# Kernel optimization log

Measured on AMD Instinct MI355X. Metric: run time of the kernel, lower is better.

Reference implementation:

```python
import jax, jax.numpy as jnp
import numpy as np

B, S, HID, NH = 4, 1024, 1024, 16
HD = HID // NH  # 64


def setup_inputs() -> dict:
    key = jax.random.key(0)
    ks = jax.random.split(key, 8)
    scale = 0.02
    return {
        "attention_mask": jnp.zeros((B, 1, 1, S), dtype=jnp.float32),
        "query": jax.random.normal(ks[0], (B, S, HID), dtype=jnp.float32),
        "key": jax.random.normal(ks[1], (B, S, HID), dtype=jnp.float32),
        "value": jax.random.normal(ks[2], (B, S, HID), dtype=jnp.float32),
        "Wq": jax.random.normal(ks[3], (HID, HID), dtype=jnp.float32) * scale,
        "bq": jnp.zeros((HID,), dtype=jnp.float32),
        "Wk": jax.random.normal(ks[4], (HID, HID), dtype=jnp.float32) * scale,
        "bk": jnp.zeros((HID,), dtype=jnp.float32),
    }


def reference(attention_mask, query, key, value, Wq, bq, Wk, bk):
    # Linear projections (torch Linear: x @ W.T + b)
    q = query @ Wq.T + bq  # [B,S,HID]
    k = key @ Wk.T + bk    # [B,S,HID]
    # split heads -> [B,NH,S,HD]
    q = q.reshape(B, S, NH, HD).transpose(0, 2, 1, 3)
    k = k.reshape(B, S, NH, HD).transpose(0, 2, 1, 3)
    scores = jnp.einsum("bhqd,bhkd->bhqk", q, k) / jnp.sqrt(jnp.float32(HD))
    scores = scores + attention_mask  # additive mask broadcast [B,1,1,S]
    probs = jax.nn.softmax(scores, axis=-1)  # [B,NH,S,S]
    # V is shared across heads; head-mean folds into a single contraction:
    # mean_h(probs_h @ V) = (sum_h probs_h) @ V / NH
    out = jnp.einsum("bhqk,bkv->bqv", probs, value) / NH  # [B,S,HID]
    return out
```

## Files before the change

kernel.cpp:

```cpp
#include <hip/hip_runtime.h>
#include <hip/hip_fp16.h>

#define B_    4
#define S_    1024
#define HID_  1024
#define NH_   16
#define HD_   64

#define LOG2E 1.44269504f
#define PSTR  40

typedef _Float16 half8 __attribute__((ext_vector_type(8)));
typedef float f32x4 __attribute__((ext_vector_type(4)));

__device__ __forceinline__ half8 cvt8(float4 a, float4 b) {
    half8 h;
    h[0] = (_Float16)a.x; h[1] = (_Float16)a.y;
    h[2] = (_Float16)a.z; h[3] = (_Float16)a.w;
    h[4] = (_Float16)b.x; h[5] = (_Float16)b.y;
    h[6] = (_Float16)b.z; h[7] = (_Float16)b.w;
    return h;
}

__global__ __launch_bounds__(512) void proj_qk_f16(
    const float* __restrict__ query, const float* __restrict__ Wq,
    const float* __restrict__ bq, _Float16* __restrict__ Oq,
    const float* __restrict__ key, const float* __restrict__ Wk,
    const float* __restrict__ bk, _Float16* __restrict__ Ok)
{
    const int f  = blockIdx.x + 8 * blockIdx.y + 256 * blockIdx.z;
    const int w2 = (f & 7) * 64 + (f >> 3);
    const int bx = w2 & 7, by = (w2 >> 3) & 31, bz = w2 >> 8;

    const float* A    = bz ? key : query;
    const float* Wm   = bz ? Wk  : Wq;
    const float* bias = bz ? bk  : bq;
    _Float16* Co      = bz ? Ok  : Oq;

    __shared__ _Float16 Al[2][128 * PSTR];
    __shared__ _Float16 Bl[2][128 * PSTR];

    const int tid  = threadIdx.x;
    const int wv   = tid >> 6;
    const int lane = tid & 63;
    const int l15  = lane & 15;
    const int quad = lane >> 4;
    const int wm   = wv & 1, wn = wv >> 1;
    const int m0   = by * 128, n0 = bx * 128;
    const int sr   = tid >> 2;
    const int sc   = (tid & 3) * 8;

    const float* ap = A  + (long)(m0 + sr) * HID_ + sc;
    const float* bp = Wm + (long)(n0 + sr) * HID_ + sc;

    f32x4 acc[4][2];
#pragma unroll
    for (int i = 0; i < 4; i++)
#pragma unroll
        for (int j = 0; j < 2; j++) acc[i][j] = (f32x4){0.f, 0.f, 0.f, 0.f};

    float4 a0 = *(const float4*)ap,       a1 = *(const float4*)(ap + 4);
    float4 b0 = *(const float4*)bp,       b1 = *(const float4*)(bp + 4);
    *(half8*)&Al[0][sr * PSTR + sc] = cvt8(a0, a1);
    *(half8*)&Bl[0][sr * PSTR + sc] = cvt8(b0, b1);
    a0 = *(const float4*)(ap + 32); a1 = *(const float4*)(ap + 36);
    b0 = *(const float4*)(bp + 32); b1 = *(const float4*)(bp + 36);
    __syncthreads();

#pragma unroll 2
    for (int kt = 0; kt < HID_; kt += 32) {
        const int p = (kt >> 5) & 1;

        float4 na0 = a0, na1 = a1, nb0 = b0, nb1 = b1;
        if (kt + 64 < HID_) {
            na0 = *(const float4*)(ap + kt + 64);
            na1 = *(const float4*)(ap + kt + 68);
            nb0 = *(const float4*)(bp + kt + 64);
            nb1 = *(const float4*)(bp + kt + 68);
        }

        half8 af[4], bfm[2];
#pragma unroll
        for (int i = 0; i < 4; i++)
            af[i] = *(const half8*)(&Al[p][(wm * 64 + i * 16 + l15) * PSTR + quad * 8]);
#pragma unroll
        for (int j = 0; j < 2; j++)
            bfm[j] = *(const half8*)(&Bl[p][(wn * 32 + j * 16 + l15) * PSTR + quad * 8]);

        if (kt + 32 < HID_) {
            *(half8*)&Al[p ^ 1][sr * PSTR + sc] = cvt8(a0, a1);
            *(half8*)&Bl[p ^ 1][sr * PSTR + sc] = cvt8(b0, b1);
        }

#pragma unroll
        for (int i = 0; i < 4; i++)
#pragma unroll
            for (int j = 0; j < 2; j++)
                acc[i][j] = __builtin_amdgcn_mfma_f32_16x16x32_f16(
                    af[i], bfm[j], acc[i][j], 0, 0, 0);

        __syncthreads();
        a0 = na0; a1 = na1; b0 = nb0; b1 = nb1;
    }

    const int isQ = (bz == 0);
#pragma unroll
    for (int j = 0; j < 2; j++) {
        int col = n0 + wn * 32 + j * 16 + l15;
        float bv = bias[col];
        int h = col >> 6, d = col & 63, p = d >> 3, jj = d & 7;
#pragma unroll
        for (int i = 0; i < 4; i++) {
            int row = m0 + wm * 64 + i * 16 + quad * 4;
            int bb = row >> 10, ss = row & 1023;
            long base;
            if (isQ)
                base = ((((long)(bb * NH_ + h) * 64 + (ss >> 4)) * 8 + p) * 16
                        + (ss & 15)) * 8 + jj;
            else
                base = (((long)(bb * NH_ + h) * 8 + p) * 1024 + ss) * 8 + jj;
#pragma unroll
            for (int r = 0; r < 4; r++)
                Co[base + r * 8] = (_Float16)(acc[i][j][r] + bv);
        }
    }
}

__global__ __launch_bounds__(512) void attn_psum_f16(
    const _Float16* __restrict__ qb,
    const _Float16* __restrict__ kb,
    const float* __restrict__ mask,
    _Float16* __restrict__ P)
{
    const int b    = blockIdx.y;
    const int qt   = blockIdx.x;
    const int q0   = qt * 16;
    const int hz   = blockIdx.z;
    const int tid  = threadIdx.x;
    const int w    = tid >> 6;
    const int lane = tid & 63;
    const int l15  = lane & 15;
    const int quad = lane >> 4;

    __shared__ float redS[2][16][8];

    const float SC = 0.125f * LOG2E;

    float mreg[8];
#pragma unroll
    for (int t = 0; t < 8; t++)
        mreg[t] = mask[b * S_ + t * 128 + w * 16 + l15] * LOG2E;

    f32x4 acc[8];
#pragma unroll
    for (int t = 0; t < 8; t++) acc[t] = (f32x4){0.f, 0.f, 0.f, 0.f};

    for (int ii = 0; ii < 4; ii++) {
        const int h = hz * 4 + ii;
        const _Float16* qh = qb + ((long)(b * NH_ + h) * 64 + qt) * 1024;
        const _Float16* kh = kb + (long)(b * NH_ + h) * 8192 * 8;

        half8 a0 = *(const half8*)(qh + quad * 128 + l15 * 8);
        half8 a1 = *(const half8*)(qh + (quad + 4) * 128 + l15 * 8);

        f32x4 s[8];
#pragma unroll
        for (int cc = 0; cc < 8; cc++) {
            const int key = cc * 128 + w * 16 + l15;
            half8 b0 = *(const half8*)(kh + (long)quad * 8192 + key * 8);
            half8 b1 = *(const half8*)(kh + (long)(quad + 4) * 8192 + key * 8);
            f32x4 c = (f32x4){0.f, 0.f, 0.f, 0.f};
            c = __builtin_amdgcn_mfma_f32_16x16x32_f16(a0, b0, c, 0, 0, 0);
            c = __builtin_amdgcn_mfma_f32_16x16x32_f16(a1, b1, c, 0, 0, 0);
            s[cc] = c;
        }

        const int p = ii & 1;
        float sm[4] = {0.f, 0.f, 0.f, 0.f};
#pragma unroll
        for (int t = 0; t < 8; t++)
#pragma unroll
            for (int r = 0; r < 4; r++) {
                float pr = exp2f(s[t][r] * SC + mreg[t]);
                s[t][r] = pr;
                sm[r] += pr;
            }
#pragma unroll
        for (int off = 1; off < 16; off <<= 1)
#pragma unroll
            for (int r = 0; r < 4; r++) sm[r] += __shfl_xor(sm[r], off);
        if (l15 == 0)
#pragma unroll
            for (int r = 0; r < 4; r++) redS[p][quad * 4 + r][w] = sm[r];
        __syncthreads();

#pragma unroll
        for (int r = 0; r < 4; r++) {
            float4 v0 = *(float4*)&redS[p][quad * 4 + r][0];
            float4 v1 = *(float4*)&redS[p][quad * 4 + r][4];
            float tot = (v0.x + v0.y + v0.z + v0.w) + (v1.x + v1.y + v1.z + v1.w);
            float inv = 1.f / tot;
#pragma unroll
            for (int t = 0; t < 8; t++) acc[t][r] += s[t][r] * inv;
        }
    }

    _Float16* prow = P + (long)hz * ((long)B_ * S_ * S_) + (long)(b * S_ + q0) * S_;
#pragma unroll
    for (int t = 0; t < 8; t++)
#pragma unroll
        for (int r = 0; r < 4; r++) {
            int row = quad * 4 + r;
            prow[(long)row * S_ + t * 128 + w * 16 + l15] = (_Float16)acc[t][r];
        }
}

__global__ __launch_bounds__(256) void vt_combine(
    const _Float16* __restrict__ P, _Float16* __restrict__ o,
    const float* __restrict__ V, _Float16* __restrict__ Vt)
{
    __shared__ float t[32][33];
    if (blockIdx.y == 0) {
        if (blockIdx.x >= 2048) return;
        const long QS = (long)B_ * S_ * S_;
        long i = (long)(blockIdx.x * 256 + threadIdx.x) * 8;
        half8 a = *(const half8*)(P + i);
        half8 b = *(const half8*)(P + QS + i);
        half8 c = *(const half8*)(P + 2 * QS + i);
        half8 d = *(const half8*)(P + 3 * QS + i);
        half8 r;
#pragma unroll
        for (int e = 0; e < 8; e++)
            r[e] = (_Float16)((float)a[e] + (float)b[e] + (float)c[e] + (float)d[e]);
        *(half8*)(o + i) = r;
    } else {
        const int x  = blockIdx.x;
        const int b  = x >> 10;
        const int s0 = ((x >> 5) & 31) * 32;
        const int h0 = (x & 31) * 32;
        const int tx = threadIdx.x & 31, ty = threadIdx.x >> 5;
#pragma unroll
        for (int rr = 0; rr < 4; rr++) {
            int s = s0 + ty + rr * 8;
            t[ty + rr * 8][tx] = V[((long)b * S_ + s) * HID_ + h0 + tx];
        }
        __syncthreads();
#pragma unroll
        for (int rr = 0; rr < 4; rr++) {
            int h = h0 + ty + rr * 8;
            Vt[((long)b * HID_ + h) * S_ + s0 + tx] = (_Float16)t[tx][ty + rr * 8];
        }
    }
}

__global__ __launch_bounds__(256) void pv_f16(
    const _Float16* __restrict__ Pc,
    const _Float16* __restrict__ Vt,
    float* __restrict__ out)
{
    const int b = blockIdx.z;
    const _Float16* A  = Pc + (long)b * S_ * S_;
    const _Float16* Bm = Vt + (long)b * HID_ * S_;

    __shared__ _Float16 Al[128 * PSTR];
    __shared__ _Float16 Bl[64 * PSTR];

    const int tid  = threadIdx.x;
    const int wv   = tid >> 6;
    const int lane = tid & 63;
    const int l15  = lane & 15;
    const int quad = lane >> 4;
    const int wm   = wv & 1, wn = wv >> 1;
    const int m0   = blockIdx.y * 128, n0 = blockIdx.x * 64;
    const int sr   = tid >> 2;
    const int sc   = (tid & 3) * 8;

    f32x4 acc[4][2];
#pragma unroll
    for (int i = 0; i < 4; i++)
#pragma unroll
        for (int j = 0; j < 2; j++) acc[i][j] = (f32x4){0.f, 0.f, 0.f, 0.f};

    for (int kt = 0; kt < S_; kt += 32) {
        half8 a0 = *(const half8*)(A  + (long)(m0 + sr) * S_ + kt + sc);
        half8 a1 = *(const half8*)(A  + (long)(m0 + 64 + sr) * S_ + kt + sc);
        half8 b0 = *(const half8*)(Bm + (long)(n0 + sr) * S_ + kt + sc);
        __syncthreads();
        *(half8*)(Al + sr * PSTR + sc) = a0;
        *(half8*)(Al + (64 + sr) * PSTR + sc) = a1;
        *(half8*)(Bl + sr * PSTR + sc) = b0;
        __syncthreads();

        half8 af[4], bfm[2];
#pragma unroll
        for (int i = 0; i < 4; i++)
            af[i] = *(const half8*)(Al + (wm * 64 + i * 16 + l15) * PSTR + quad * 8);
#pragma unroll
        for (int j = 0; j < 2; j++)
            bfm[j] = *(const half8*)(Bl + (wn * 32 + j * 16 + l15) * PSTR + quad * 8);
#pragma unroll
        for (int i = 0; i < 4; i++)
#pragma unroll
            for (int j = 0; j < 2; j++)
                acc[i][j] = __builtin_amdgcn_mfma_f32_16x16x32_f16(
                    af[i], bfm[j], acc[i][j], 0, 0, 0);
    }

    const float alpha = 1.f / NH_;
#pragma unroll
    for (int i = 0; i < 4; i++) {
        int row = m0 + wm * 64 + i * 16 + quad * 4;
#pragma unroll
        for (int j = 0; j < 2; j++) {
            int col = n0 + wn * 32 + j * 16 + l15;
#pragma unroll
            for (int r = 0; r < 4; r++)
                out[(long)(b * S_ + row + r) * HID_ + col] = acc[i][j][r] * alpha;
        }
    }
}

extern "C" void kernel_launch(void* const* d_in, const int* in_sizes, int n_in,
                              void* d_out, int out_size, void* d_ws, size_t ws_size,
                              hipStream_t stream)
{
    const float* mask  = (const float*)d_in[0];
    const float* query = (const float*)d_in[1];
    const float* key   = (const float*)d_in[2];
    const float* value = (const float*)d_in[3];
    const float* Wq    = (const float*)d_in[4];
    const float* bq    = (const float*)d_in[5];
    const float* Wk    = (const float*)d_in[6];
    const float* bk    = (const float*)d_in[7];
    float* out = (float*)d_out;

    char* ws = (char*)d_ws;
    const long MB = 1l << 20;
    _Float16* qbuf = (_Float16*)(ws);
    _Float16* kbuf = (_Float16*)(ws + 8 * MB);
    _Float16* Pq   = (_Float16*)(ws + 16 * MB);
    _Float16* Vt   = (_Float16*)(ws);
    _Float16* psum = (_Float16*)(ws + 8 * MB);

    proj_qk_f16<<<dim3(HID_ / 128, (B_ * S_) / 128, 2), dim3(512), 0, stream>>>(
        query, Wq, bq, qbuf, key, Wk, bk, kbuf);

    attn_psum_f16<<<dim3(S_ / 16, B_, 4), dim3(512), 0, stream>>>(
        qbuf, kbuf, mask, Pq);

    vt_combine<<<dim3(4096, 2), dim3(256), 0, stream>>>(Pq, psum, value, Vt);

    pv_f16<<<dim3(HID_ / 64, S_ / 128, B_), dim3(256), 0, stream>>>(psum, Vt, out);
}
```

Baseline: 209.8 us.

## Fuse head-group partial sum into PV GEMM with double-buffered LDS pipeline

Removes the separate combine pass that summed four per-head-group probability partials into psum, and instead sums the four partials on the fly while loading A tiles inside pv_f16. The PV GEMM also gains double-buffered LDS with register prefetch one tile ahead and a swizzled block ordering for L2 locality. __syncthreads is replaced by a custom barrier (lgkmcnt wait + s_barrier + sched_barrier) in both GEMMs. The intent is to drop the 8MB-write plus re-read round trip of the combined matrix. The cost is that every PV tile now re-reads four fp16 partials per element, and each of the 16 column blocks reads them again, which raises global traffic and register pressure.

Result: slower. 221.1 us (+5.4%).

```diff
diff --git a/kernel.cpp b/kernel.cpp
--- a/kernel.cpp
+++ b/kernel.cpp
@@ -20,6 +20,12 @@
     h[4] = (_Float16)b.x; h[5] = (_Float16)b.y;
     h[6] = (_Float16)b.z; h[7] = (_Float16)b.w;
     return h;
+}
+
+__device__ __forceinline__ void lds_barrier() {
+    asm volatile("s_waitcnt lgkmcnt(0)" ::: "memory");
+    __builtin_amdgcn_s_barrier();
+    __builtin_amdgcn_sched_barrier(0);
 }
 
 __global__ __launch_bounds__(512) void proj_qk_f16(
@@ -65,7 +71,7 @@
     *(half8*)&Bl[0][sr * PSTR + sc] = cvt8(b0, b1);
     a0 = *(const float4*)(ap + 32); a1 = *(const float4*)(ap + 36);
     b0 = *(const float4*)(bp + 32); b1 = *(const float4*)(bp + 36);
-    __syncthreads();
+    lds_barrier();
 
 #pragma unroll 2
     for (int kt = 0; kt < HID_; kt += 32) {
@@ -99,7 +105,7 @@
                 acc[i][j] = __builtin_amdgcn_mfma_f32_16x16x32_f16(
                     af[i], bfm[j], acc[i][j], 0, 0, 0);
 
-        __syncthreads();
+        lds_barrier();
         a0 = na0; a1 = na1; b0 = nb0; b1 = nb1;
     }
 
@@ -215,55 +221,44 @@
         }
 }
 
-__global__ __launch_bounds__(256) void vt_combine(
-    const _Float16* __restrict__ P, _Float16* __restrict__ o,
+__global__ __launch_bounds__(256) void v_transpose(
     const float* __restrict__ V, _Float16* __restrict__ Vt)
 {
     __shared__ float t[32][33];
-    if (blockIdx.y == 0) {
-        if (blockIdx.x >= 2048) return;
-        const long QS = (long)B_ * S_ * S_;
-        long i = (long)(blockIdx.x * 256 + threadIdx.x) * 8;
-        half8 a = *(const half8*)(P + i);
-        half8 b = *(const half8*)(P + QS + i);
-        half8 c = *(const half8*)(P + 2 * QS + i);
-        half8 d = *(const half8*)(P + 3 * QS + i);
-        half8 r;
-#pragma unroll
-        for (int e = 0; e < 8; e++)
-            r[e] = (_Float16)((float)a[e] + (float)b[e] + (float)c[e] + (float)d[e]);
-        *(half8*)(o + i) = r;
-    } else {
-        const int x  = blockIdx.x;
-        const int b  = x >> 10;
-        const int s0 = ((x >> 5) & 31) * 32;
-        const int h0 = (x & 31) * 32;
-        const int tx = threadIdx.x & 31, ty = threadIdx.x >> 5;
-#pragma unroll
-        for (int rr = 0; rr < 4; rr++) {
-            int s = s0 + ty + rr * 8;
-            t[ty + rr * 8][tx] = V[((long)b * S_ + s) * HID_ + h0 + tx];
-        }
-        __syncthreads();
-#pragma unroll
-        for (int rr = 0; rr < 4; rr++) {
-            int h = h0 + ty + rr * 8;
-            Vt[((long)b * HID_ + h) * S_ + s0 + tx] = (_Float16)t[tx][ty + rr * 8];
-        }
+    const int x  = blockIdx.x;
+    const int b  = x >> 10;
+    const int s0 = ((x >> 5) & 31) * 32;
+    const int h0 = (x & 31) * 32;
+    const int tx = threadIdx.x & 31, ty = threadIdx.x >> 5;
+#pragma unroll
+    for (int rr = 0; rr < 4; rr++) {
+        int s = s0 + ty + rr * 8;
+        t[ty + rr * 8][tx] = V[((long)b * S_ + s) * HID_ + h0 + tx];
+    }
+    __syncthreads();
+#pragma unroll
+    for (int rr = 0; rr < 4; rr++) {
+        int h = h0 + ty + rr * 8;
+        Vt[((long)b * HID_ + h) * S_ + s0 + tx] = (_Float16)t[tx][ty + rr * 8];
     }
 }
 
 __global__ __launch_bounds__(256) void pv_f16(
-    const _Float16* __restrict__ Pc,
+    const _Float16* __restrict__ P,
     const _Float16* __restrict__ Vt,
     float* __restrict__ out)
 {
-    const int b = blockIdx.z;
-    const _Float16* A  = Pc + (long)b * S_ * S_;
+    const int f  = blockIdx.x + 16 * blockIdx.y + 128 * blockIdx.z;
+    const int w2 = (f & 7) * 64 + (f >> 3);
+    const int bx = w2 & 15, by = (w2 >> 4) & 7, bz = w2 >> 7;
+
+    const int b = bz;
+    const long QS = (long)B_ * S_ * S_;
+    const _Float16* A  = P  + (long)b * S_ * S_;
     const _Float16* Bm = Vt + (long)b * HID_ * S_;
 
-    __shared__ _Float16 Al[128 * PSTR];
-    __shared__ _Float16 Bl[64 * PSTR];
+    __shared__ _Float16 Al[2][128 * PSTR];
+    __shared__ _Float16 Bl[2][64 * PSTR];
 
     const int tid  = threadIdx.x;
     const int wv   = tid >> 6;
@@ -271,7 +266,7 @@
     const int l15  = lane & 15;
     const int quad = lane >> 4;
     const int wm   = wv & 1, wn = wv >> 1;
-    const int m0   = blockIdx.y * 128, n0 = blockIdx.x * 64;
+    const int m0   = by * 128, n0 = bx * 64;
     const int sr   = tid >> 2;
     const int sc   = (tid & 3) * 8;
 
@@ -281,29 +276,77 @@
 #pragma unroll
         for (int j = 0; j < 2; j++) acc[i][j] = (f32x4){0.f, 0.f, 0.f, 0.f};
 
+    half8 ca[2][4], cb;
+
+#pragma unroll
+    for (int r = 0; r < 2; r++) {
+        const _Float16* p0 = A + (long)(m0 + r * 64 + sr) * S_ + sc;
+        half8 x0 = *(const half8*)(p0);
+        half8 x1 = *(const half8*)(p0 + QS);
+        half8 x2 = *(const half8*)(p0 + 2 * QS);
+        half8 x3 = *(const half8*)(p0 + 3 * QS);
+        *(half8*)&Al[0][(r * 64 + sr) * PSTR + sc] = (x0 + x1) + (x2 + x3);
+    }
+    *(half8*)&Bl[0][sr * PSTR + sc] = *(const half8*)(Bm + (long)(n0 + sr) * S_ + sc);
+#pragma unroll
+    for (int r = 0; r < 2; r++)
+#pragma unroll
+        for (int q = 0; q < 4; q++)
+            ca[r][q] = *(const half8*)(A + (long)q * QS + (long)(m0 + r * 64 + sr) * S_ + 32 + sc);
+    cb = *(const half8*)(Bm + (long)(n0 + sr) * S_ + 32 + sc);
+    lds_barrier();
+
+#pragma unroll 2
     for (int kt = 0; kt < S_; kt += 32) {
-        half8 a0 = *(const half8*)(A  + (long)(m0 + sr) * S_ + kt + sc);
-        half8 a1 = *(const half8*)(A  + (long)(m0 + 64 + sr) * S_ + kt + sc);
-        half8 b0 = *(const half8*)(Bm + (long)(n0 + sr) * S_ + kt + sc);
-        __syncthreads();
-        *(half8*)(Al + sr * PSTR + sc) = a0;
-        *(half8*)(Al + (64 + sr) * PSTR + sc) = a1;
-        *(half8*)(Bl + sr * PSTR + sc) = b0;
-        __syncthreads();
+        const int p = (kt >> 5) & 1;
+
+        half8 na[2][4], nb;
+        if (kt + 64 < S_) {
+#pragma unroll
+            for (int r = 0; r < 2; r++)
+#pragma unroll
+                for (int q = 0; q < 4; q++)
+                    na[r][q] = *(const half8*)(A + (long)q * QS
+                        + (long)(m0 + r * 64 + sr) * S_ + kt + 64 + sc);
+            nb = *(const half8*)(Bm + (long)(n0 + sr) * S_ + kt + 64 + sc);
+        } else {
+#pragma unroll
+            for (int r = 0; r < 2; r++)
+#pragma unroll
+                for (int q = 0; q < 4; q++) na[r][q] = ca[r][q];
+            nb = cb;
+        }
 
         half8 af[4], bfm[2];
 #pragma unroll
         for (int i = 0; i < 4; i++)
-            af[i] = *(const half8*)(Al + (wm * 64 + i * 16 + l15) * PSTR + quad * 8);
+            af[i] = *(const half8*)(&Al[p][(wm * 64 + i * 16 + l15) * PSTR + quad * 8]);
 #pragma unroll
         for (int j = 0; j < 2; j++)
-            bfm[j] = *(const half8*)(Bl + (wn * 32 + j * 16 + l15) * PSTR + quad * 8);
+            bfm[j] = *(const half8*)(&Bl[p][(wn * 32 + j * 16 + l15) * PSTR + quad * 8]);
+
+        if (kt + 32 < S_) {
+#pragma unroll
+            for (int r = 0; r < 2; r++) {
+                half8 s = (ca[r][0] + ca[r][1]) + (ca[r][2] + ca[r][3]);
+                *(half8*)&Al[p ^ 1][(r * 64 + sr) * PSTR + sc] = s;
+            }
+            *(half8*)&Bl[p ^ 1][sr * PSTR + sc] = cb;
+        }
+
 #pragma unroll
         for (int i = 0; i < 4; i++)
 #pragma unroll
             for (int j = 0; j < 2; j++)
                 acc[i][j] = __builtin_amdgcn_mfma_f32_16x16x32_f16(
                     af[i], bfm[j], acc[i][j], 0, 0, 0);
+
+        lds_barrier();
+#pragma unroll
+        for (int r = 0; r < 2; r++)
+#pragma unroll
+            for (int q = 0; q < 4; q++) ca[r][q] = na[r][q];
+        cb = nb;
     }
 
     const float alpha = 1.f / NH_;
@@ -340,7 +383,6 @@
     _Float16* kbuf = (_Float16*)(ws + 8 * MB);
     _Float16* Pq   = (_Float16*)(ws + 16 * MB);
     _Float16* Vt   = (_Float16*)(ws);
-    _Float16* psum = (_Float16*)(ws + 8 * MB);
 
     proj_qk_f16<<<dim3(HID_ / 128, (B_ * S_) / 128, 2), dim3(512), 0, stream>>>(
         query, Wq, bq, qbuf, key, Wk, bk, kbuf);
@@ -348,7 +390,7 @@
     attn_psum_f16<<<dim3(S_ / 16, B_, 4), dim3(512), 0, stream>>>(
         qbuf, kbuf, mask, Pq);
 
-    vt_combine<<<dim3(4096, 2), dim3(256), 0, stream>>>(Pq, psum, value, Vt);
-
-    pv_f16<<<dim3(HID_ / 64, S_ / 128, B_), dim3(256), 0, stream>>>(psum, Vt, out);
-}
+    v_transpose<<<dim3(4096), dim3(256), 0, stream>>>(value, Vt);
+
+    pv_f16<<<dim3(HID_ / 64, S_ / 128, B_), dim3(256), 0, stream>>>(Pq, Vt, out);
+}
```

## Double-buffer PV GEMM, add XCD-aware block swizzles, lighter barriers and fast exp2

Applied to the files above, without the earlier changes.

The PV GEMM is rewritten to double-buffer its LDS tiles and register-prefetch global loads two steps ahead, with one barrier per k-step instead of two. This lets global loads overlap the MFMA work. Block indices in the attention and PV kernels are remapped so blocks sharing a batch land on the same XCD, aiming for better L2 reuse. Barriers now wait only on LDS counters, and exp2 uses the raw hardware instruction with an fma, trading a little accuracy and some scheduling freedom.

Result: faster. 196.1 us (-6.5%).

```diff
diff --git a/kernel.cpp b/kernel.cpp
--- a/kernel.cpp
+++ b/kernel.cpp
@@ -20,6 +20,22 @@
     h[4] = (_Float16)b.x; h[5] = (_Float16)b.y;
     h[6] = (_Float16)b.z; h[7] = (_Float16)b.w;
     return h;
+}
+
+__device__ __forceinline__ float fexp2(float x) {
+#if __has_builtin(__builtin_amdgcn_exp2f)
+    return __builtin_amdgcn_exp2f(x);
+#else
+    float r;
+    asm("v_exp_f32 %0, %1\n\ts_nop 0" : "=v"(r) : "v"(x));
+    return r;
+#endif
+}
+
+__device__ __forceinline__ void lds_barrier() {
+    asm volatile("s_waitcnt lgkmcnt(0)" ::: "memory");
+    __builtin_amdgcn_s_barrier();
+    __builtin_amdgcn_sched_barrier(0);
 }
 
 __global__ __launch_bounds__(512) void proj_qk_f16(
@@ -65,7 +81,7 @@
     *(half8*)&Bl[0][sr * PSTR + sc] = cvt8(b0, b1);
     a0 = *(const float4*)(ap + 32); a1 = *(const float4*)(ap + 36);
     b0 = *(const float4*)(bp + 32); b1 = *(const float4*)(bp + 36);
-    __syncthreads();
+    lds_barrier();
 
 #pragma unroll 2
     for (int kt = 0; kt < HID_; kt += 32) {
@@ -99,7 +115,7 @@
                 acc[i][j] = __builtin_amdgcn_mfma_f32_16x16x32_f16(
                     af[i], bfm[j], acc[i][j], 0, 0, 0);
 
-        __syncthreads();
+        lds_barrier();
         a0 = na0; a1 = na1; b0 = nb0; b1 = nb1;
     }
 
@@ -132,10 +148,13 @@
     const float* __restrict__ mask,
     _Float16* __restrict__ P)
 {
-    const int b    = blockIdx.y;
-    const int qt   = blockIdx.x;
+    const int f   = blockIdx.x + 64 * blockIdx.y + 256 * blockIdx.z;
+    const int w2s = (f & 7) * 128 + (f >> 3);
+    const int qt  = w2s & 63;
+    const int b   = (w2s >> 6) & 3;
+    const int hz  = w2s >> 8;
+
     const int q0   = qt * 16;
-    const int hz   = blockIdx.z;
     const int tid  = threadIdx.x;
     const int w    = tid >> 6;
     const int lane = tid & 63;
@@ -181,7 +200,7 @@
         for (int t = 0; t < 8; t++)
 #pragma unroll
             for (int r = 0; r < 4; r++) {
-                float pr = exp2f(s[t][r] * SC + mreg[t]);
+                float pr = fexp2(fmaf(s[t][r], SC, mreg[t]));
                 s[t][r] = pr;
                 sm[r] += pr;
             }
@@ -258,12 +277,17 @@
     const _Float16* __restrict__ Vt,
     float* __restrict__ out)
 {
-    const int b = blockIdx.z;
+    const int f   = blockIdx.x + 16 * blockIdx.y + 128 * blockIdx.z;
+    const int xcd = f & 7, ii = f >> 3;
+    const int bx  = ii & 15;
+    const int by  = (ii >> 4) + ((xcd & 1) << 2);
+    const int b   = xcd >> 1;
+
     const _Float16* A  = Pc + (long)b * S_ * S_;
     const _Float16* Bm = Vt + (long)b * HID_ * S_;
 
-    __shared__ _Float16 Al[128 * PSTR];
-    __shared__ _Float16 Bl[64 * PSTR];
+    __shared__ _Float16 Al[2][128 * PSTR];
+    __shared__ _Float16 Bl[2][64 * PSTR];
 
     const int tid  = threadIdx.x;
     const int wv   = tid >> 6;
@@ -271,39 +295,65 @@
     const int l15  = lane & 15;
     const int quad = lane >> 4;
     const int wm   = wv & 1, wn = wv >> 1;
-    const int m0   = blockIdx.y * 128, n0 = blockIdx.x * 64;
+    const int m0   = by * 128, n0 = bx * 64;
     const int sr   = tid >> 2;
     const int sc   = (tid & 3) * 8;
 
+    const _Float16* ap0 = A  + (long)(m0 + sr) * S_ + sc;
+    const _Float16* ap1 = A  + (long)(m0 + 64 + sr) * S_ + sc;
+    const _Float16* bp0 = Bm + (long)(n0 + sr) * S_ + sc;
+
     f32x4 acc[4][2];
 #pragma unroll
     for (int i = 0; i < 4; i++)
 #pragma unroll
         for (int j = 0; j < 2; j++) acc[i][j] = (f32x4){0.f, 0.f, 0.f, 0.f};
 
+    half8 ca0 = *(const half8*)(ap0);
+    half8 ca1 = *(const half8*)(ap1);
+    half8 cb0 = *(const half8*)(bp0);
+    *(half8*)&Al[0][sr * PSTR + sc] = ca0;
+    *(half8*)&Al[0][(64 + sr) * PSTR + sc] = ca1;
+    *(half8*)&Bl[0][sr * PSTR + sc] = cb0;
+    ca0 = *(const half8*)(ap0 + 32);
+    ca1 = *(const half8*)(ap1 + 32);
+    cb0 = *(const half8*)(bp0 + 32);
+    lds_barrier();
+
+#pragma unroll 2
     for (int kt = 0; kt < S_; kt += 32) {
-        half8 a0 = *(const half8*)(A  + (long)(m0 + sr) * S_ + kt + sc);
-        half8 a1 = *(const half8*)(A  + (long)(m0 + 64 + sr) * S_ + kt + sc);
-        half8 b0 = *(const half8*)(Bm + (long)(n0 + sr) * S_ + kt + sc);
-        __syncthreads();
-        *(half8*)(Al + sr * PSTR + sc) = a0;
-        *(half8*)(Al + (64 + sr) * PSTR + sc) = a1;
-        *(half8*)(Bl + sr * PSTR + sc) = b0;
-        __syncthreads();
+        const int p = (kt >> 5) & 1;
+
+        half8 na0 = ca0, na1 = ca1, nb0 = cb0;
+        if (kt + 64 < S_) {
+            na0 = *(const half8*)(ap0 + kt + 64);
+            na1 = *(const half8*)(ap1 + kt + 64);
+            nb0 = *(const half8*)(bp0 + kt + 64);
+        }
 
         half8 af[4], bfm[2];
 #pragma unroll
         for (int i = 0; i < 4; i++)
-            af[i] = *(const half8*)(Al + (wm * 64 + i * 16 + l15) * PSTR + quad * 8);
+            af[i] = *(const half8*)(&Al[p][(wm * 64 + i * 16 + l15) * PSTR + quad * 8]);
 #pragma unroll
         for (int j = 0; j < 2; j++)
-            bfm[j] = *(const half8*)(Bl + (wn * 32 + j * 16 + l15) * PSTR + quad * 8);
+            bfm[j] = *(const half8*)(&Bl[p][(wn * 32 + j * 16 + l15) * PSTR + quad * 8]);
+
+        if (kt + 32 < S_) {
+            *(half8*)&Al[p ^ 1][sr * PSTR + sc] = ca0;
+            *(half8*)&Al[p ^ 1][(64 + sr) * PSTR + sc] = ca1;
+            *(half8*)&Bl[p ^ 1][sr * PSTR + sc] = cb0;
+        }
+
 #pragma unroll
         for (int i = 0; i < 4; i++)
 #pragma unroll
             for (int j = 0; j < 2; j++)
                 acc[i][j] = __builtin_amdgcn_mfma_f32_16x16x32_f16(
                     af[i], bfm[j], acc[i][j], 0, 0, 0);
+
+        lds_barrier();
+        ca0 = na0; ca1 = na1; cb0 = nb0;
     }
 
     const float alpha = 1.f / NH_;
```
